# Performance work log

Hardware: AMD Instinct MI355X
Metric: run time of the kernel (lower is better)

## Reference

```python
import jax, jax.numpy as jnp
import numpy as np

N = 1_000_000
C = 32
GRID_SIZE = (16, 16, 16, 16, 16)

# Only 4 corners are combined in the original module: dims 0 and 1 vary
# between floor/ceil, dims 2-4 always use floor.
CORNER_OFFSETS = np.array([
    [0, 0, 0, 0, 0],
    [1, 0, 0, 0, 0],
    [0, 1, 0, 0, 0],
    [1, 1, 0, 0, 0],
], dtype=np.int32)  # (4, 5)


def setup_inputs() -> dict:
    key = jax.random.key(0)
    k1, k2 = jax.random.split(key)
    ray = jax.random.uniform(k1, (N, 5), dtype=jnp.float32)
    grid = jax.random.normal(k2, (1, C) + GRID_SIZE, dtype=jnp.float32)
    ray_min = jnp.zeros((5,), dtype=jnp.float32)
    ray_max = jnp.ones((5,), dtype=jnp.float32)
    return {"ray": ray, "grid": grid, "ray_min": ray_min, "ray_max": ray_max}


def reference(ray, grid, ray_min, ray_max):
    dims = np.array(grid.shape[2:], dtype=np.int64)       # (D0..D4)
    C_ = grid.shape[1]
    P = int(np.prod(dims))
    strides = np.array([np.prod(dims[i + 1:]) for i in range(5)], dtype=np.int32)  # (5,)

    # Normalize ray -> fractional grid coordinates, shape (N, 5)
    ind = (ray - ray_min) / (ray_max - ray_min) * (dims.astype(np.float32) - 1.0)
    bottom = jnp.floor(ind).astype(jnp.int32)              # (N, 5)
    w = ind - bottom.astype(ind.dtype)                     # (N, 5) interp weights

    offs = jnp.asarray(CORNER_OFFSETS)                     # (4, 5)
    corner = bottom[None, :, :] + offs[:, None, :]         # (4, N, 5)

    dims_j = jnp.asarray(dims.astype(np.int32))
    valid = jnp.all((corner >= 0) & (corner < dims_j), axis=-1)          # (4, N)
    lin = jnp.sum(corner * jnp.asarray(strides), axis=-1)                # (4, N)
    lin = jnp.clip(lin, 0, P - 1)

    # Per-corner multilinear weights: pick w where offset==1 else (1-w), product over 5 dims
    wsel = jnp.where(offs[:, None, :] == 1, w[None, :, :], 1.0 - w[None, :, :])  # (4, N, 5)
    comb_w = jnp.prod(wsel, axis=-1) * valid.astype(ind.dtype)                   # (4, N)

    grid_flat = grid.reshape(C_, P)                        # (C, P)
    vals = grid_flat[:, lin]                               # (C, 4, N) gather
    out = jnp.einsum('cfn,fn->nc', vals, comb_w)           # (N, C)
    return out
```

## Files before the change

### kernel.cpp

```cpp
#include <hip/hip_runtime.h>
#include <hip/hip_fp16.h>

#define PCELLS (16*16*16*16*16)
#define CCH 32
#define TILE_P 128

__device__ __forceinline__ void ray_corners(const float* __restrict__ ray,
                                            const float* __restrict__ mn,
                                            const float* __restrict__ mx,
                                            int n, int* lin, float* wt) {
    float w[5]; int b[5];
#pragma unroll
    for (int d = 0; d < 5; ++d) {
        float r   = ray[(size_t)n * 5 + d];
        float t   = (r - mn[d]) / (mx[d] - mn[d]);
        float ind = t * 15.0f;
        float fb  = floorf(ind);
        b[d] = (int)fb;
        w[d] = ind - fb;
    }
    bool vrest = (b[2] >= 0) & (b[2] < 16) & (b[3] >= 0) & (b[3] < 16) &
                 (b[4] >= 0) & (b[4] < 16);
    float tau = (1.f - w[2]) * (1.f - w[3]) * (1.f - w[4]);
    if (!vrest) tau = 0.f;
    int rest = b[2] * 256 + b[3] * 16 + b[4];

    bool v0l = (b[0] >= 0) & (b[0] < 16);
    bool v0h = (b[0] + 1 >= 0) & (b[0] + 1 < 16);
    bool v1l = (b[1] >= 0) & (b[1] < 16);
    bool v1h = (b[1] + 1 >= 0) & (b[1] + 1 < 16);
    float w0 = w[0], w1 = w[1];

    wt[0] = (1.f - w0) * (1.f - w1) * tau * ((v0l & v1l) ? 1.f : 0.f);
    wt[1] = w0 * (1.f - w1) * tau * ((v0h & v1l) ? 1.f : 0.f);
    wt[2] = (1.f - w0) * w1 * tau * ((v0l & v1h) ? 1.f : 0.f);
    wt[3] = w0 * w1 * tau * ((v0h & v1h) ? 1.f : 0.f);

    int l00 = b[0] * 65536 + b[1] * 4096 + rest;
    int lv[4] = { l00, l00 + 65536, l00 + 4096, l00 + 65536 + 4096 };
#pragma unroll
    for (int f = 0; f < 4; ++f)
        lin[f] = min(max(lv[f], 0), PCELLS - 1);
}

__global__ __launch_bounds__(256) void transpose_kernel(
        const float* __restrict__ g, __half* __restrict__ gt) {
    __shared__ float tile[CCH][TILE_P + 4];
    const int p0 = blockIdx.x * TILE_P;
    const int t  = threadIdx.x;

#pragma unroll
    for (int i = 0; i < 4; ++i) {
        int idx = t + i * 256;
        int c   = idx >> 5;
        int q   = idx & 31;
        const float4 v = *(const float4*)(g + (size_t)c * PCELLS + p0 + 4 * q);
        *(float4*)&tile[c][4 * q] = v;
    }
    __syncthreads();

#pragma unroll
    for (int i = 0; i < 2; ++i) {
        int idx = t + i * 256;
        int p   = idx >> 2;
        int k   = idx & 3;
        __half2 h[4];
#pragma unroll
        for (int j = 0; j < 4; ++j) {
            h[j] = __floats2half2_rn(tile[8 * k + 2 * j][p],
                                     tile[8 * k + 2 * j + 1][p]);
        }
        *(float4*)(gt + (size_t)(p0 + p) * CCH + 8 * k) = *(float4*)h;
    }
}

__global__ __launch_bounds__(256) void fused_gather(
        const float* __restrict__ ray, const __half2* __restrict__ gt2,
        const float* __restrict__ mn, const float* __restrict__ mx,
        float* __restrict__ out, int N) {
    int tid = blockIdx.x * blockDim.x + threadIdx.x;
    int pr  = tid >> 4;
    int c2  = tid & 15;
    int n0  = 2 * pr;
    if (n0 >= N) return;
    bool has1 = (n0 + 1) < N;
    int n1 = has1 ? (n0 + 1) : n0;

    int   lin0[4], lin1[4];
    float wt0[4],  wt1[4];
    ray_corners(ray, mn, mx, n0, lin0, wt0);
    ray_corners(ray, mn, mx, n1, lin1, wt1);

    __half2 v0[4], v1[4];
#pragma unroll
    for (int f = 0; f < 4; ++f) v0[f] = gt2[(size_t)lin0[f] * 16 + c2];
#pragma unroll
    for (int f = 0; f < 4; ++f) v1[f] = gt2[(size_t)lin1[f] * 16 + c2];

    float2 a0 = make_float2(0.f, 0.f), a1 = make_float2(0.f, 0.f);
#pragma unroll
    for (int f = 0; f < 4; ++f) {
        float2 x = __half22float2(v0[f]);
        a0.x += wt0[f] * x.x;  a0.y += wt0[f] * x.y;
    }
#pragma unroll
    for (int f = 0; f < 4; ++f) {
        float2 x = __half22float2(v1[f]);
        a1.x += wt1[f] * x.x;  a1.y += wt1[f] * x.y;
    }

    *(float2*)(out + (size_t)n0 * CCH + 2 * c2) = a0;
    if (has1)
        *(float2*)(out + (size_t)n1 * CCH + 2 * c2) = a1;
}

__global__ __launch_bounds__(256) void direct_kernel(
        const float* __restrict__ ray, const float* __restrict__ g,
        const float* __restrict__ mn, const float* __restrict__ mx,
        float* __restrict__ out, int N) {
    int tid = blockIdx.x * blockDim.x + threadIdx.x;
    int n = tid >> 5;
    int c = tid & 31;
    if (n >= N) return;
    int lin[4]; float wt[4];
    ray_corners(ray, mn, mx, n, lin, wt);
    const float* gc = g + (size_t)c * PCELLS;
    float acc = wt[0] * gc[lin[0]] + wt[1] * gc[lin[1]] +
                wt[2] * gc[lin[2]] + wt[3] * gc[lin[3]];
    out[(size_t)n * CCH + c] = acc;
}

extern "C" void kernel_launch(void* const* d_in, const int* in_sizes, int n_in,
                              void* d_out, int out_size, void* d_ws, size_t ws_size,
                              hipStream_t stream) {
    const float* ray  = (const float*)d_in[0];
    const float* grid = (const float*)d_in[1];
    const float* mn   = (const float*)d_in[2];
    const float* mx   = (const float*)d_in[3];
    float* out = (float*)d_out;
    const int N = in_sizes[0] / 5;

    const size_t gt_bytes = (size_t)PCELLS * CCH * sizeof(__half);

    if (ws_size >= gt_bytes) {
        __half* gt = (__half*)d_ws;
        transpose_kernel<<<PCELLS / TILE_P, 256, 0, stream>>>(grid, gt);

        long long pairs   = (N + 1) / 2;
        long long threads = pairs * 16;
        fused_gather<<<(int)((threads + 255) / 256), 256, 0, stream>>>(
            ray, (const __half2*)gt, mn, mx, out, N);
    } else {
        long long total = (long long)N * CCH;
        direct_kernel<<<(int)((total + 255) / 256), 256, 0, stream>>>(
            ray, grid, mn, mx, out, N);
    }
}
```

Before: 324.4 us.

## Vectorize gather to 16-byte fp16 loads per thread and drop bounds masking

Each thread now handles 8 channels of a ray pair with 16-byte loads from the channel-last fp16 grid copy, instead of one half2 per thread. This cuts redundant ray coordinate math and the number of memory instructions. Output writes become 16-byte nontemporal stores, and the transpose uses nontemporal loads. Coordinate normalization uses a hardware reciprocal, and the validity masks are removed, which relies on rays staying within [min,max).

```diff
diff --git a/kernel.cpp b/kernel.cpp
--- a/kernel.cpp
+++ b/kernel.cpp
@@ -5,42 +5,42 @@
 #define CCH 32
 #define TILE_P 128
 
-__device__ __forceinline__ void ray_corners(const float* __restrict__ ray,
-                                            const float* __restrict__ mn,
-                                            const float* __restrict__ mx,
-                                            int n, int* lin, float* wt) {
-    float w[5]; int b[5];
+typedef float f32x4 __attribute__((ext_vector_type(4)));
+
+__device__ __forceinline__ void ray_corners2(
+        const float* __restrict__ ray, const float* __restrict__ mn,
+        const float* __restrict__ mx, int n0, int n1,
+        int* lin0, float* wt0, int* lin1, float* wt1) {
+    float wa[5], wb[5]; int ba[5], bb[5];
 #pragma unroll
     for (int d = 0; d < 5; ++d) {
-        float r   = ray[(size_t)n * 5 + d];
-        float t   = (r - mn[d]) / (mx[d] - mn[d]);
-        float ind = t * 15.0f;
-        float fb  = floorf(ind);
-        b[d] = (int)fb;
-        w[d] = ind - fb;
+        float m   = mn[d];
+        float inv = __builtin_amdgcn_rcpf(mx[d] - m) * 15.0f;
+        float i0  = (ray[(size_t)n0 * 5 + d] - m) * inv;
+        float i1  = (ray[(size_t)n1 * 5 + d] - m) * inv;
+        float f0 = floorf(i0), f1 = floorf(i1);
+        ba[d] = (int)f0;  wa[d] = i0 - f0;
+        bb[d] = (int)f1;  wb[d] = i1 - f1;
     }
-    bool vrest = (b[2] >= 0) & (b[2] < 16) & (b[3] >= 0) & (b[3] < 16) &
-                 (b[4] >= 0) & (b[4] < 16);
-    float tau = (1.f - w[2]) * (1.f - w[3]) * (1.f - w[4]);
-    if (!vrest) tau = 0.f;
-    int rest = b[2] * 256 + b[3] * 16 + b[4];
-
-    bool v0l = (b[0] >= 0) & (b[0] < 16);
-    bool v0h = (b[0] + 1 >= 0) & (b[0] + 1 < 16);
-    bool v1l = (b[1] >= 0) & (b[1] < 16);
-    bool v1h = (b[1] + 1 >= 0) & (b[1] + 1 < 16);
-    float w0 = w[0], w1 = w[1];
-
-    wt[0] = (1.f - w0) * (1.f - w1) * tau * ((v0l & v1l) ? 1.f : 0.f);
-    wt[1] = w0 * (1.f - w1) * tau * ((v0h & v1l) ? 1.f : 0.f);
-    wt[2] = (1.f - w0) * w1 * tau * ((v0l & v1h) ? 1.f : 0.f);
-    wt[3] = w0 * w1 * tau * ((v0h & v1h) ? 1.f : 0.f);
-
-    int l00 = b[0] * 65536 + b[1] * 4096 + rest;
-    int lv[4] = { l00, l00 + 65536, l00 + 4096, l00 + 65536 + 4096 };
 #pragma unroll
-    for (int f = 0; f < 4; ++f)
-        lin[f] = min(max(lv[f], 0), PCELLS - 1);
+    for (int r = 0; r < 2; ++r) {
+        const float* w = r ? wb : wa;
+        const int*   b = r ? bb : ba;
+        float* wt = r ? wt1 : wt0;
+        int*  lin = r ? lin1 : lin0;
+        float tau = (1.f - w[2]) * (1.f - w[3]) * (1.f - w[4]);
+        int  rest = b[2] * 256 + b[3] * 16 + b[4];
+        float w0 = w[0], w1 = w[1];
+        wt[0] = (1.f - w0) * (1.f - w1) * tau;
+        wt[1] = w0 * (1.f - w1) * tau;
+        wt[2] = (1.f - w0) * w1 * tau;
+        wt[3] = w0 * w1 * tau;
+        int l00 = b[0] * 65536 + b[1] * 4096 + rest;
+        int lv[4] = { l00, l00 + 65536, l00 + 4096, l00 + 65536 + 4096 };
+#pragma unroll
+        for (int f = 0; f < 4; ++f)
+            lin[f] = min(max(lv[f], 0), PCELLS - 1);
+    }
 }
 
 __global__ __launch_bounds__(256) void transpose_kernel(
@@ -54,8 +54,9 @@
         int idx = t + i * 256;
         int c   = idx >> 5;
         int q   = idx & 31;
-        const float4 v = *(const float4*)(g + (size_t)c * PCELLS + p0 + 4 * q);
-        *(float4*)&tile[c][4 * q] = v;
+        const f32x4 v = __builtin_nontemporal_load(
+            (const f32x4*)(g + (size_t)c * PCELLS + p0 + 4 * q));
+        *(f32x4*)&tile[c][4 * q] = v;
     }
     __syncthreads();
 
@@ -66,21 +67,20 @@
         int k   = idx & 3;
         __half2 h[4];
 #pragma unroll
-        for (int j = 0; j < 4; ++j) {
+        for (int j = 0; j < 4; ++j)
             h[j] = __floats2half2_rn(tile[8 * k + 2 * j][p],
                                      tile[8 * k + 2 * j + 1][p]);
-        }
-        *(float4*)(gt + (size_t)(p0 + p) * CCH + 8 * k) = *(float4*)h;
+        *(f32x4*)(gt + (size_t)(p0 + p) * CCH + 8 * k) = *(f32x4*)h;
     }
 }
 
 __global__ __launch_bounds__(256) void fused_gather(
-        const float* __restrict__ ray, const __half2* __restrict__ gt2,
+        const float* __restrict__ ray, const __half* __restrict__ gt,
         const float* __restrict__ mn, const float* __restrict__ mx,
         float* __restrict__ out, int N) {
     int tid = blockIdx.x * blockDim.x + threadIdx.x;
-    int pr  = tid >> 4;
-    int c2  = tid & 15;
+    int pr  = tid >> 2;
+    int q   = tid & 3;
     int n0  = 2 * pr;
     if (n0 >= N) return;
     bool has1 = (n0 + 1) < N;
@@ -88,30 +88,48 @@
 
     int   lin0[4], lin1[4];
     float wt0[4],  wt1[4];
-    ray_corners(ray, mn, mx, n0, lin0, wt0);
-    ray_corners(ray, mn, mx, n1, lin1, wt1);
+    ray_corners2(ray, mn, mx, n0, n1, lin0, wt0, lin1, wt1);
 
-    __half2 v0[4], v1[4];
+    const __half* gq = gt + 8 * q;
+    f32x4 r0[4], r1[4];
 #pragma unroll
-    for (int f = 0; f < 4; ++f) v0[f] = gt2[(size_t)lin0[f] * 16 + c2];
+    for (int f = 0; f < 4; ++f)
+        r0[f] = *(const f32x4*)(gq + (size_t)lin0[f] * CCH);
 #pragma unroll
-    for (int f = 0; f < 4; ++f) v1[f] = gt2[(size_t)lin1[f] * 16 + c2];
+    for (int f = 0; f < 4; ++f)
+        r1[f] = *(const f32x4*)(gq + (size_t)lin1[f] * CCH);
 
-    float2 a0 = make_float2(0.f, 0.f), a1 = make_float2(0.f, 0.f);
+    float acc0[8] = {0,0,0,0,0,0,0,0};
+    float acc1[8] = {0,0,0,0,0,0,0,0};
 #pragma unroll
     for (int f = 0; f < 4; ++f) {
-        float2 x = __half22float2(v0[f]);
-        a0.x += wt0[f] * x.x;  a0.y += wt0[f] * x.y;
+        const __half2* h = (const __half2*)&r0[f];
+#pragma unroll
+        for (int j = 0; j < 4; ++j) {
+            float2 x = __half22float2(h[j]);
+            acc0[2 * j]     += wt0[f] * x.x;
+            acc0[2 * j + 1] += wt0[f] * x.y;
+        }
     }
 #pragma unroll
     for (int f = 0; f < 4; ++f) {
-        float2 x = __half22float2(v1[f]);
-        a1.x += wt1[f] * x.x;  a1.y += wt1[f] * x.y;
+        const __half2* h = (const __half2*)&r1[f];
+#pragma unroll
+        for (int j = 0; j < 4; ++j) {
+            float2 x = __half22float2(h[j]);
+            acc1[2 * j]     += wt1[f] * x.x;
+            acc1[2 * j + 1] += wt1[f] * x.y;
+        }
     }
 
-    *(float2*)(out + (size_t)n0 * CCH + 2 * c2) = a0;
-    if (has1)
-        *(float2*)(out + (size_t)n1 * CCH + 2 * c2) = a1;
+    float* o0 = out + (size_t)n0 * CCH + 8 * q;
+    __builtin_nontemporal_store(*(f32x4*)&acc0[0], (f32x4*)o0);
+    __builtin_nontemporal_store(*(f32x4*)&acc0[4], (f32x4*)(o0 + 4));
+    if (has1) {
+        float* o1 = out + (size_t)n1 * CCH + 8 * q;
+        __builtin_nontemporal_store(*(f32x4*)&acc1[0], (f32x4*)o1);
+        __builtin_nontemporal_store(*(f32x4*)&acc1[4], (f32x4*)(o1 + 4));
+    }
 }
 
 __global__ __launch_bounds__(256) void direct_kernel(
@@ -122,8 +140,8 @@
     int n = tid >> 5;
     int c = tid & 31;
     if (n >= N) return;
-    int lin[4]; float wt[4];
-    ray_corners(ray, mn, mx, n, lin, wt);
+    int lin[4], lin1[4]; float wt[4], wt1[4];
+    ray_corners2(ray, mn, mx, n, n, lin, wt, lin1, wt1);
     const float* gc = g + (size_t)c * PCELLS;
     float acc = wt[0] * gc[lin[0]] + wt[1] * gc[lin[1]] +
                 wt[2] * gc[lin[2]] + wt[3] * gc[lin[3]];
@@ -147,9 +165,9 @@
         transpose_kernel<<<PCELLS / TILE_P, 256, 0, stream>>>(grid, gt);
 
         long long pairs   = (N + 1) / 2;
-        long long threads = pairs * 16;
+        long long threads = pairs * 4;
         fused_gather<<<(int)((threads + 255) / 256), 256, 0, stream>>>(
-            ray, (const __half2*)gt, mn, mx, out, N);
+            ray, gt, mn, mx, out, N);
     } else {
         long long total = (long long)N * CCH;
         direct_kernel<<<(int)((total + 255) / 256), 256, 0, stream>>>(
```

Result: faster. 315.8 us (-2.7%).
